# Kernel tuning notes

Hardware: AMD Instinct MI355X
Metric: run time of the kernel (lower is better)

## Reference

```python
import jax, jax.numpy as jnp
import numpy as np

INF = 1e30  # sentinel for 'unreached' cost
MAX_ITERS = 512


def setup_inputs() -> dict:
    key = jax.random.key(0)
    img = jax.random.uniform(key, (3, 2048, 2048), dtype=jnp.float32)
    return {"img": img}


def _sobel_mag(gray):
    # gray: [H,W] -> gradient magnitude [H,W] (the 'processing_filter')
    kx = jnp.array([[-1.0, 0.0, 1.0], [-2.0, 0.0, 2.0], [-1.0, 0.0, 1.0]], gray.dtype)
    k = jnp.stack([kx, kx.T])[:, None]  # [2,1,3,3]
    g = jax.lax.conv_general_dilated(gray[None, None], k, (1, 1), 'SAME')[0]  # [2,H,W]
    return jnp.sqrt(g[0] ** 2 + g[1] ** 2)


def _neighbor_min(c):
    # min over 4-connected neighbors, INF padding at borders
    big_r = jnp.full((1, c.shape[1]), INF, c.dtype)
    big_c = jnp.full((c.shape[0], 1), INF, c.dtype)
    n = jnp.concatenate([big_r, c[:-1]], 0)
    s = jnp.concatenate([c[1:], big_r], 0)
    w = jnp.concatenate([big_c, c[:, :-1]], 1)
    e = jnp.concatenate([c[:, 1:], big_c], 1)
    return jnp.minimum(jnp.minimum(n, s), jnp.minimum(w, e))


def _relax(cost, img):
    # minimax-path (flood-level) relaxation: cost[p] = min(cost[p], max(min_nbr_cost, img[p]))
    return jnp.minimum(cost, jnp.maximum(_neighbor_min(cost), img))


def _watershed2(img, markers):
    # marker-based watershed on topography `img` with labels {1,2}.
    # Label of p = argmin over seed sets of the minimax path cost (flooding level),
    # which matches skimage.segmentation.watershed region assignment (4-connectivity).
    c1 = jnp.where(markers == 1, img, jnp.float32(INF))
    c2 = jnp.where(markers == 2, img, jnp.float32(INF))

    def cond(st):
        _, _, i, ch = st
        return jnp.logical_and(ch, i < MAX_ITERS)

    def body(st):
        c1, c2, i, _ = st
        n1 = _relax(c1, img)
        n2 = _relax(c2, img)
        ch = jnp.logical_or(jnp.any(n1 < c1), jnp.any(n2 < c2))
        return n1, n2, i + 1, ch

    c1, c2, _, _ = jax.lax.while_loop(cond, body, (c1, c2, jnp.int32(0), jnp.bool_(True)))
    return jnp.where(c2 < c1, jnp.float32(2.0), jnp.float32(1.0))


def _forward(img):
    gray = jnp.einsum('chw,c->hw', img, jnp.array([0.2989, 0.587, 0.114], img.dtype))
    filter_res = _sobel_mag(gray)  # [H,W]
    q_hi = jnp.quantile(filter_res, 0.9925)
    q_lo = jnp.quantile(filter_res, 0.9825)
    # torch sets 2 first, then 1, so pixels satisfying both end up as 1
    markers = jnp.where(filter_res <= q_lo, 1, jnp.where(filter_res >= q_hi, 2, 0))
    labels = _watershed2(gray, markers)[None]  # [1,H,W], values in {1,2}
    labels = labels - labels.min()
    return labels / labels.max()


def reference(img):
    return _forward(img)
```

## Files before the change

kernel.cpp:

```cpp
#include <hip/hip_runtime.h>
#include <hip/hip_cooperative_groups.h>

#define HH 2048
#define WW 2048
#define NPX (HH*WW)
#define INFV 1e30f
#define TS 128
#define NT 16
#define NTL 256
#define CY 128

namespace cg = cooperative_groups;

__device__ __forceinline__ void BARL(){
  __builtin_amdgcn_sched_barrier(0);
  asm volatile("s_waitcnt lgkmcnt(0)" ::: "memory");
  __builtin_amdgcn_s_barrier();
  __builtin_amdgcn_sched_barrier(0);
}

__device__ __forceinline__ float sobel_at(const float* __restrict__ g, int y, int x){
  float a00,a01,a02,a10,a12,a20,a21,a22;
  if (y>0 && y<HH-1 && x>0 && x<WW-1){
    const float* p = g + (size_t)(y-1)*WW + x;
    a00=p[-1]; a01=p[0]; a02=p[1];
    p += WW;   a10=p[-1];          a12=p[1];
    p += WW;   a20=p[-1]; a21=p[0]; a22=p[1];
  } else {
    auto at=[&](int yy,int xx)->float{
      return (yy<0||yy>=HH||xx<0||xx>=WW)?0.0f:g[(size_t)yy*WW+xx];
    };
    a00=at(y-1,x-1); a01=at(y-1,x); a02=at(y-1,x+1);
    a10=at(y,  x-1);                a12=at(y,  x+1);
    a20=at(y+1,x-1); a21=at(y+1,x); a22=at(y+1,x+1);
  }
  float gx = __fadd_rn(__fadd_rn(__fsub_rn(a02,a00), __fmul_rn(2.0f,__fsub_rn(a12,a10))), __fsub_rn(a22,a20));
  float gy = __fadd_rn(__fadd_rn(__fsub_rn(a20,a00), __fmul_rn(2.0f,__fsub_rn(a21,a01))), __fsub_rn(a22,a02));
  return sqrtf(__fadd_rn(__fmul_rn(gx,gx),__fmul_rn(gy,gy)));
}

__global__ void gray_kernel(const float* __restrict__ img, float* __restrict__ gray){
  const float* R=img; const float* G=img+NPX; const float* B=img+2*(size_t)NPX;
  for (int i=blockIdx.x*blockDim.x+threadIdx.x; i<NPX; i+=gridDim.x*blockDim.x){
    gray[i] = __fadd_rn(__fadd_rn(__fmul_rn(0.2989f,R[i]),__fmul_rn(0.587f,G[i])),__fmul_rn(0.114f,B[i]));
  }
}

__global__ void sobel_hist1(const float* __restrict__ gray, float* __restrict__ fr,
                            unsigned* __restrict__ hist){
  __shared__ unsigned h[4*2048];
  for (int i=threadIdx.x;i<4*2048;i+=blockDim.x) h[i]=0;
  __syncthreads();
  const int rep=(threadIdx.x&3)*2048;
  for (int i=blockIdx.x*blockDim.x+threadIdx.x; i<NPX; i+=gridDim.x*blockDim.x){
    int y=i>>11, x=i&(WW-1);
    float f=sobel_at(gray,y,x);
    fr[i]=f;
    unsigned key=__float_as_uint(f);
    atomicAdd(&h[rep+(key>>21)],1u);
  }
  __syncthreads();
  for (int i=threadIdx.x;i<2048;i+=blockDim.x){
    unsigned s=h[i]+h[i+2048]+h[i+4096]+h[i+6144];
    if (s) atomicAdd(&hist[i],s);
  }
}

__global__ void hist_l2(const float* __restrict__ fr, const unsigned* __restrict__ sel1,
                        unsigned* __restrict__ hist2){
  __shared__ unsigned h[4*2048];
  __shared__ unsigned sb[4];
  if (threadIdx.x<4) sb[threadIdx.x]=sel1[threadIdx.x];
  for (int i=threadIdx.x;i<4*2048;i+=blockDim.x) h[i]=0;
  __syncthreads();
  for (int i=blockIdx.x*blockDim.x+threadIdx.x; i<NPX; i+=gridDim.x*blockDim.x){
    unsigned key=__float_as_uint(fr[i]);
    unsigned b=key>>21, sub=(key>>10)&0x7FFu;
    #pragma unroll
    for (int k=0;k<4;++k) if (b==sb[k]) atomicAdd(&h[k*2048+sub],1u);
  }
  __syncthreads();
  for (int i=threadIdx.x;i<4*2048;i+=blockDim.x){ unsigned s=h[i]; if (s) atomicAdd(&hist2[i],s); }
}

__global__ void hist_l3(const float* __restrict__ fr, const unsigned* __restrict__ sel1,
                        const unsigned* __restrict__ sel2, unsigned* __restrict__ hist3){
  __shared__ unsigned h[4*1024];
  __shared__ unsigned pf[4];
  if (threadIdx.x<4) pf[threadIdx.x]=(sel1[threadIdx.x]<<11)|sel2[threadIdx.x];
  for (int i=threadIdx.x;i<4*1024;i+=blockDim.x) h[i]=0;
  __syncthreads();
  for (int i=blockIdx.x*blockDim.x+threadIdx.x; i<NPX; i+=gridDim.x*blockDim.x){
    unsigned key=__float_as_uint(fr[i]);
    unsigned p22=key>>10, sub=key&0x3FFu;
    #pragma unroll
    for (int k=0;k<4;++k) if (p22==pf[k]) atomicAdd(&h[k*1024+sub],1u);
  }
  __syncthreads();
  for (int i=threadIdx.x;i<4*1024;i+=blockDim.x){ unsigned s=h[i]; if (s) atomicAdd(&hist3[i],s); }
}

__global__ void scan_l1(const unsigned* __restrict__ hist, unsigned* __restrict__ sel1,
                        unsigned* __restrict__ rem1){
  __shared__ unsigned part[1024];
  const int t=threadIdx.x;
  unsigned a=hist[2*t], b=hist[2*t+1];
  part[t]=a+b; __syncthreads();
  for (int off=1;off<1024;off<<=1){
    unsigned add=(t>=off)?part[t-off]:0u; __syncthreads();
    part[t]+=add; __syncthreads();
  }
  unsigned before=(t>0)?part[t-1]:0u;
  const unsigned R[4]={4120902u,4120903u,4162845u,4162846u};
  unsigned cum=before;
  #pragma unroll
  for (int i=0;i<4;++i) if (R[i]>=cum && R[i]<cum+a){ sel1[i]=2*t;   rem1[i]=R[i]-cum; }
  cum+=a;
  #pragma unroll
  for (int i=0;i<4;++i) if (R[i]>=cum && R[i]<cum+b){ sel1[i]=2*t+1; rem1[i]=R[i]-cum; }
}

__global__ void scan_l2(const unsigned* __restrict__ hist2, const unsigned* __restrict__ rem1,
                        unsigned* __restrict__ sel2, unsigned* __restrict__ rem2){
  __shared__ unsigned part[1024];
  const int t=threadIdx.x;
  for (int i=0;i<4;++i){
    const unsigned* hh=hist2+i*2048;
    unsigned a=hh[2*t], b=hh[2*t+1];
    part[t]=a+b; __syncthreads();
    for (int off=1;off<1024;off<<=1){
      unsigned add=(t>=off)?part[t-off]:0u; __syncthreads();
      part[t]+=add; __syncthreads();
    }
    unsigned before=(t>0)?part[t-1]:0u;
    unsigned r=rem1[i], cum=before;
    if (r>=cum && r<cum+a){ sel2[i]=2*t;   rem2[i]=r-cum; }
    cum+=a;
    if (r>=cum && r<cum+b){ sel2[i]=2*t+1; rem2[i]=r-cum; }
    __syncthreads();
  }
}

__global__ void scan_l3(const unsigned* __restrict__ hist3, const unsigned* __restrict__ sel1,
                        const unsigned* __restrict__ sel2, const unsigned* __restrict__ rem2,
                        float* __restrict__ scal){
  __shared__ unsigned part[1024];
  __shared__ float vals[4];
  const int t=threadIdx.x;
  for (int i=0;i<4;++i){
    unsigned c=hist3[i*1024+t];
    part[t]=c; __syncthreads();
    for (int off=1;off<1024;off<<=1){
      unsigned add=(t>=off)?part[t-off]:0u; __syncthreads();
      part[t]+=add; __syncthreads();
    }
    unsigned before=(t>0)?part[t-1]:0u;
    unsigned r=rem2[i];
    if (r>=before && r<before+c){
      unsigned key=(sel1[i]<<21)|(sel2[i]<<10)|(unsigned)t;
      vals[i]=__uint_as_float(key);
    }
    __syncthreads();
  }
  if (t==0){
    scal[0]=__fadd_rn(__fmul_rn(vals[0],0.25f),__fmul_rn(vals[1],0.75f));
    scal[1]=__fadd_rn(__fmul_rn(vals[2],0.25f),__fmul_rn(vals[3],0.75f));
  }
}

__global__ void init_cost(const float* __restrict__ gray, const float* frbuf,
                          const float* __restrict__ scal,
                          float* c1out, float* __restrict__ c2out){
  const float qlo=scal[0], qhi=scal[1];
  for (int i=blockIdx.x*blockDim.x+threadIdx.x; i<NPX; i+=gridDim.x*blockDim.x){
    float f=frbuf[i];
    float g=gray[i];
    bool m1 = (f<=qlo);
    bool m2 = (!m1) && (f>=qhi);
    c1out[i] = m1 ? g : INFV;
    c2out[i] = (m1|m2) ? g : INFV;
  }
}


#define HSCAN_LR(va,vb,gA,gB,hl) do{ \
  float ql_=gA[j], qh_=va[j]; \
  qh_=fminf(vb[j],fmaxf(gB[j],qh_)); ql_=fmaxf(gB[j],ql_); \
  _Pragma("unroll") \
  for (int d_=1;d_<64;d_<<=1){ \
    float pl_=__shfl_up(ql_,(unsigned)d_), ph_=__shfl_up(qh_,(unsigned)d_); \
    if (c>=d_){ qh_=fminf(qh_,fmaxf(ql_,ph_)); ql_=fmaxf(ql_,pl_); } \
  } \
  float E_=fminf(qh_,fmaxf(ql_,(hl))); \
  float In_=__shfl_up(E_,1u); if(c==0) In_=(hl); \
  float na_=fminf(va[j],fmaxf(gA[j],In_)); if(na_<va[j]){va[j]=na_;ch=true;} \
  float nb_=fminf(vb[j],fmaxf(gB[j],na_)); if(nb_<vb[j]){vb[j]=nb_;ch=true;} \
}while(0)

#define HSCAN_RL(va,vb,gA,gB,hr) do{ \
  float ql_=gB[j], qh_=vb[j]; \
  qh_=fminf(va[j],fmaxf(gA[j],qh_)); ql_=fmaxf(gA[j],ql_); \
  _Pragma("unroll") \
  for (int d_=1;d_<64;d_<<=1){ \
    float pl_=__shfl_down(ql_,(unsigned)d_), ph_=__shfl_down(qh_,(unsigned)d_); \
    if (c+d_<64){ qh_=fminf(qh_,fmaxf(ql_,ph_)); ql_=fmaxf(ql_,pl_); } \
  } \
  float E_=fminf(qh_,fmaxf(ql_,(hr))); \
  float In_=__shfl_down(E_,1u); if(c==63) In_=(hr); \
  float nb_=fminf(vb[j],fmaxf(gB[j],In_)); if(nb_<vb[j]){vb[j]=nb_;ch=true;} \
  float na_=fminf(va[j],fmaxf(gA[j],nb_)); if(na_<va[j]){va[j]=na_;ch=true;} \
}while(0)

#define VCOMP_DN(va,gA,Larr,Harr,XX) { float ql_=gA[0], qh_=va[0]; \
  _Pragma("unroll") for (int jj_=1;jj_<8;++jj_){ qh_=fminf(va[jj_],fmaxf(gA[jj_],qh_)); ql_=fmaxf(gA[jj_],ql_);} \
  Larr[w][XX]=ql_; Harr[w][XX]=qh_; }

#define VCOMP_UP(va,gA,Larr,Harr,XX) { float ql_=gA[7], qh_=va[7]; \
  _Pragma("unroll") for (int jj_=6;jj_>=0;--jj_){ qh_=fminf(va[jj_],fmaxf(gA[jj_],qh_)); ql_=fmaxf(gA[jj_],ql_);} \
  Larr[w][XX]=ql_; Harr[w][XX]=qh_; }

#define VAPPLY_DN(va,gA,Larr,XX) { float In_=Larr[w][XX]; \
  _Pragma("unroll") for (int jj_=0;jj_<8;++jj_){ float nv_=fminf(va[jj_],fmaxf(In_,gA[jj_])); if(nv_<va[jj_]){va[jj_]=nv_;ch=true;} In_=nv_; } }

#define VAPPLY_UP(va,gA,Larr,XX) { float In_=Larr[w][XX]; \
  _Pragma("unroll") for (int jj_=7;jj_>=0;--jj_){ float nv_=fminf(va[jj_],fmaxf(In_,gA[jj_])); if(nv_<va[jj_]){va[jj_]=nv_;ch=true;} In_=nv_; } }

#define CHAIN_DN(Harr,Larr,HT) { float E=HALO[HT][x]; \
  _Pragma("unroll") for (int b_=0;b_<16;++b_){ float I=E; E=fminf(Harr[b_][x],fmaxf(Larr[b_][x],I)); Larr[b_][x]=I; } }

#define CHAIN_UP(Harr,Larr,HB) { float E=HALO[HB][x]; \
  _Pragma("unroll") for (int b_=15;b_>=0;--b_){ float I=E; E=fminf(Harr[b_][x],fmaxf(Larr[b_][x],I)); Larr[b_][x]=I; } }

#define HFIELD(va,vb,IHL,IHR) do{ \
  _Pragma("unroll") \
  for (int j=0;j<8;++j){ \
    const int r_=(w<<3)|j; \
    const float hl=HALO[IHL][r_], hr=HALO[IHR][r_]; \
    { float la_=__shfl_up(vb[j],1u); if(c==0) la_=hl; \
      bool p_=__any((fminf(va[j],fmaxf(la_,ga[j]))<va[j])||(fminf(vb[j],fmaxf(va[j],gb[j]))<vb[j])); \
      if (p_){ HSCAN_LR(va,vb,ga,gb,hl); } } \
    { float ra_=__shfl_down(va[j],1u); if(c==63) ra_=hr; \
      bool p_=__any((fminf(vb[j],fmaxf(ra_,gb[j]))<vb[j])||(fminf(va[j],fmaxf(vb[j],ga[j]))<va[j])); \
      if (p_){ HSCAN_RL(va,vb,ga,gb,hr); } } \
  } \
}while(0)

#define ASTORE(p,v) __hip_atomic_store((p),(v),__ATOMIC_RELAXED,__HIP_MEMORY_SCOPE_AGENT)
#define ALOAD(p)    __hip_atomic_load((p),__ATOMIC_RELAXED,__HIP_MEMORY_SCOPE_AGENT)

#define CYCLE(HV,CUR,NXT) do{ \
  if (hsrc){ \
    if (HV < HALO[harr][hx]){ \
      HALO[harr][hx]=HV; \
      if (harr<4){ if (harr&1) VN2[NXT]=1; else VN1[NXT]=1; } \
      else       { if (harr&1) HN2[NXT]=1; else HN1[NXT]=1; } \
    } \
    HV=ALOAD(hsrc); \
  } \
  const int vn1=VN1[CUR], hn1=HN1[CUR], vn2=VN2[CUR], hn2=HN2[CUR]; \
  if (!(vn1|hn1|vn2|hn2)){ \
    BARL(); \
  } else { \
    if (vn1){ \
      VCOMP_DN(v1a,ga,DNL1,DNH1,x0) VCOMP_DN(v1b,gb,DNL1,DNH1,x0+1) \
      VCOMP_UP(v1a,ga,UPL1,UPH1,x0) VCOMP_UP(v1b,gb,UPL1,UPH1,x0+1) \
    } \
    if (vn2){ \
      VCOMP_DN(v2a,ga,DNL2,DNH2,x0) VCOMP_DN(v2b,gb,DNL2,DNH2,x0+1) \
      VCOMP_UP(v2a,ga,UPL2,UPH2,x0) VCOMP_UP(v2b,gb,UPL2,UPH2,x0+1) \
    } \
    BARL(); \
    if (w<8){ \
      const int x=((w&1)<<6)|c; \
      const bool go = (w>>2) ? (vn2!=0) : (vn1!=0); \
      if (go){ \
        switch(w>>1){ \
          case 0: CHAIN_DN(DNH1,DNL1,0) break; \
          case 1: CHAIN_UP(UPH1,UPL1,2) break; \
          case 2: CHAIN_DN(DNH2,DNL2,1) break; \
          default:CHAIN_UP(UPH2,UPL2,3) break; \
        } \
      } \
    } \
    BARL(); \
    bool chf1=false, chf2=false; \
    if (vn1){ bool ch=false; \
      VAPPLY_DN(v1a,ga,DNL1,x0) VAPPLY_DN(v1b,gb,DNL1,x0+1) \
      VAPPLY_UP(v1a,ga,UPL1,x0) VAPPLY_UP(v1b,gb,UPL1,x0+1) \
      if (ch){ chf1=true; HN1[NXT]=1; } \
    } \
    if (hn1){ bool ch=false; \
      HFIELD(v1a,v1b,4,6); \
      if (ch){ chf1=true; VN1[NXT]=1; } \
    } \
    if (vn2){ bool ch=false; \
      VAPPLY_DN(v2a,ga,DNL2,x0) VAPPLY_DN(v2b,gb,DNL2,x0+1) \
      VAPPLY_UP(v2a,ga,UPL2,x0) VAPPLY_UP(v2b,gb,UPL2,x0+1) \
      if (ch){ chf2=true; HN2[NXT]=1; } \
    } \
    if (hn2){ bool ch=false; \
      HFIELD(v2a,v2b,5,7); \
      if (ch){ chf2=true; VN2[NXT]=1; } \
    } \
    if (chf1|chf2){ \
      if (w==0){ const int eb=(tile*4+0)*128; \
        if(chf1){ ASTORE(EB1+eb+x0,v1a[0]); ASTORE(EB1+eb+x0+1,v1b[0]); } \
        if(chf2){ ASTORE(EB2+eb+x0,v2a[0]); ASTORE(EB2+eb+x0+1,v2b[0]); } } \
      if (w==15){ const int eb=(tile*4+1)*128; \
        if(chf1){ ASTORE(EB1+eb+x0,v1a[7]); ASTORE(EB1+eb+x0+1,v1b[7]); } \
        if(chf2){ ASTORE(EB2+eb+x0,v2a[7]); ASTORE(EB2+eb+x0+1,v2b[7]); } } \
      if (c==0){ const int eb=(tile*4+2)*128+(w<<3); \
        _Pragma("unroll") \
        for (int j=0;j<8;++j){ if(chf1)ASTORE(EB1+eb+j,v1a[j]); if(chf2)ASTORE(EB2+eb+j,v2a[j]); } } \
      if (c==63){ const int eb=(tile*4+3)*128+(w<<3); \
        _Pragma("unroll") \
        for (int j=0;j<8;++j){ if(chf1)ASTORE(EB1+eb+j,v1b[j]); if(chf2)ASTORE(EB2+eb+j,v2b[j]); } } \
      wflag=1; \
    } \
    if (tid==0){ VN1[CUR]=0; HN1[CUR]=0; VN2[CUR]=0; HN2[CUR]=0; } \
    BARL(); \
  } \
}while(0)

__global__ void __launch_bounds__(1024,4)
ws_solve(float* __restrict__ c1g, const float* __restrict__ grayg, float* outg,
         int* __restrict__ flagIt)
{
  __shared__ float DNL1[16][128], DNH1[16][128], DNL2[16][128], DNH2[16][128];
  __shared__ float UPL1[16][128], UPH1[16][128], UPL2[16][128], UPH2[16][128];
  __shared__ float HALO[8][128];
  __shared__ int VN1[2],HN1[2],VN2[2],HN2[2];
  __shared__ int wflag;
  cg::grid_group grid = cg::this_grid();
  const int tid=threadIdx.x, w=tid>>6, c=tid&63;
  const int xcd=blockIdx.x&7, idx=blockIdx.x>>3;
  const int tx=((xcd&3)<<2)|(idx&3), ty=((xcd>>2)<<3)|(idx>>2);
  const int tile=ty*NT+tx;
  const int by=ty*TS, bx=tx*TS, x0=c<<1;
  float* EB1=outg;
  float* EB2=outg+(NTL*4*128);

  const int hx=tid&127, harr=tid>>7;
  const float* hsrc=nullptr;
  {
    const float* EB=(harr&1)?EB2:EB1;
    switch(harr>>1){
      case 0: if (ty>0)    hsrc=EB+((tile-NT)*4+1)*128+hx; break;
      case 1: if (ty<NT-1) hsrc=EB+((tile+NT)*4+0)*128+hx; break;
      case 2: if (tx>0)    hsrc=EB+((tile-1)*4+3)*128+hx;  break;
      default:if (tx<NT-1) hsrc=EB+((tile+1)*4+2)*128+hx;  break;
    }
  }

  float v1a[8],v1b[8],v2a[8],v2b[8],ga[8],gb[8];
  {
    size_t base=(size_t)(by+(w<<3))*WW + bx + x0;
    #pragma unroll
    for (int j=0;j<8;++j){
      float2 t1=*(const float2*)(c1g+base);
      float2 t2=*(const float2*)(outg+base);
      float2 tg=*(const float2*)(grayg+base);
      v1a[j]=t1.x; v1b[j]=t1.y; v2a[j]=t2.x; v2b[j]=t2.y; ga[j]=tg.x; gb[j]=tg.y;
      base+=(size_t)WW;
    }
  }
  grid.sync();

  if (w==0){ const int eb=(tile*4+0)*128;
    ASTORE(EB1+eb+x0,v1a[0]); ASTORE(EB1+eb+x0+1,v1b[0]);
    ASTORE(EB2+eb+x0,v2a[0]); ASTORE(EB2+eb+x0+1,v2b[0]); }
  if (w==15){ const int eb=(tile*4+1)*128;
    ASTORE(EB1+eb+x0,v1a[7]); ASTORE(EB1+eb+x0+1,v1b[7]);
    ASTORE(EB2+eb+x0,v2a[7]); ASTORE(EB2+eb+x0+1,v2b[7]); }
  if (c==0){ const int eb=(tile*4+2)*128+(w<<3);
    #pragma unroll
    for (int j=0;j<8;++j){ ASTORE(EB1+eb+j,v1a[j]); ASTORE(EB2+eb+j,v2a[j]); } }
  if (c==63){ const int eb=(tile*4+3)*128+(w<<3);
    #pragma unroll
    for (int j=0;j<8;++j){ ASTORE(EB1+eb+j,v1b[j]); ASTORE(EB2+eb+j,v2b[j]); } }
  HALO[harr][hx]=INFV;
  if (tid==0){ VN1[0]=1;HN1[0]=1;VN2[0]=1;HN2[0]=1;
               VN1[1]=0;HN1[1]=0;VN2[1]=0;HN2[1]=0; wflag=0; }
  __threadfence();
  grid.sync();

  float hvA=INFV, hvB=INFV;
  if (hsrc){ hvA=ALOAD(hsrc); hvB=ALOAD(hsrc); }

  for (int win=0; win<48; ++win){
    for (int cyc=0; cyc<CY; cyc+=2){
      CYCLE(hvA,0,1);
      CYCLE(hvB,1,0);
    }
    if (tid==0 && wflag) atomicMax(flagIt,win+1);
    __threadfence();
    grid.sync();
    int fv=ALOAD(flagIt);
    if (fv<=win) break;
    if (tid==0) wflag=0;
    __syncthreads();
  }
  {
    size_t base=(size_t)(by+(w<<3))*WW + bx + x0;
    #pragma unroll
    for (int j=0;j<8;++j){
      float2 o; o.x=(v2a[j]<v1a[j])?1.0f:0.0f; o.y=(v2b[j]<v1b[j])?1.0f:0.0f;
      *(float2*)(outg+base)=o;
      base+=(size_t)WW;
    }
  }
}

extern "C" void kernel_launch(void* const* d_in, const int* in_sizes, int n_in,
                              void* d_out, int out_size, void* d_ws, size_t ws_size,
                              hipStream_t stream)
{
  const float* img=(const float*)d_in[0];
  float* out=(float*)d_out;
  char* wsb=(char*)d_ws;
  float* gray=(float*)wsb;
  float* c1  =(float*)(wsb + (size_t)NPX*4);
  unsigned* meta=(unsigned*)(wsb + (size_t)NPX*8);
  float* c2 = out;

  unsigned* hist1=meta;
  unsigned* hist2=meta+2048;
  unsigned* hist3=meta+10240;
  unsigned* sel1 =meta+14336;
  unsigned* rem1 =meta+14340;
  unsigned* sel2 =meta+14344;
  unsigned* rem2 =meta+14348;
  float*    scal =(float*)(meta+14352);
  int*      flagIt=(int*)(meta+14354);

  hipMemsetAsync(meta, 0, 14355*sizeof(unsigned), stream);
  hipLaunchKernelGGL(gray_kernel, dim3(4096), dim3(256), 0, stream, img, gray);
  hipLaunchKernelGGL(sobel_hist1, dim3(1024), dim3(256), 0, stream, gray, c1, hist1);
  hipLaunchKernelGGL(scan_l1, dim3(1), dim3(1024), 0, stream, hist1, sel1, rem1);
  hipLaunchKernelGGL(hist_l2, dim3(1024), dim3(256), 0, stream, c1, sel1, hist2);
  hipLaunchKernelGGL(scan_l2, dim3(1), dim3(1024), 0, stream, hist2, rem1, sel2, rem2);
  hipLaunchKernelGGL(hist_l3, dim3(1024), dim3(256), 0, stream, c1, sel1, sel2, hist3);
  hipLaunchKernelGGL(scan_l3, dim3(1), dim3(1024), 0, stream, hist3, sel1, sel2, rem2, scal);
  hipLaunchKernelGGL(init_cost, dim3(4096), dim3(256), 0, stream, gray, c1, scal, c1, c2);

  void* args[]={ (void*)&c1,(void*)&gray,(void*)&out,(void*)&flagIt };
  (void)hipLaunchCooperativeKernel(ws_solve, dim3(NTL), dim3(1024), args, 0, stream);
}
```

Measured before the change: 609.5 us.

## Add overlapping-tile local pre-solve pass before cooperative watershed flood

Adds a non-cooperative tile_solve kernel that loads 128x128 windows with 32-pixel overlap, runs up to 64 local relaxation cycles in shared memory and registers, and writes back the central 64x64 region. The aim is to converge most of the cost field locally before the cooperative grid-synchronized solver runs. It also shrinks the cycles per window (CY 128 to 32) and raises the window cap, so the grid-wide convergence check fires more often. The cost is an extra full-image kernel pass with redundant halo work. The write-back also relies on the local minimax values staying valid upper bounds, which they do because they are still real path costs.

```diff
diff --git a/kernel.cpp b/kernel.cpp
--- a/kernel.cpp
+++ b/kernel.cpp
@@ -8,7 +8,7 @@
 #define TS 128
 #define NT 16
 #define NTL 256
-#define CY 128
+#define CY 32
 
 namespace cg = cooperative_groups;
 
@@ -247,6 +247,103 @@
 
 #define ASTORE(p,v) __hip_atomic_store((p),(v),__ATOMIC_RELAXED,__HIP_MEMORY_SCOPE_AGENT)
 #define ALOAD(p)    __hip_atomic_load((p),__ATOMIC_RELAXED,__HIP_MEMORY_SCOPE_AGENT)
+
+__global__ void __launch_bounds__(1024,4)
+tile_solve(float* __restrict__ c1g, float* __restrict__ cg, const float* __restrict__ grayg)
+{
+  __shared__ float DNL1[16][128], DNH1[16][128], DNL2[16][128], DNH2[16][128];
+  __shared__ float UPL1[16][128], UPH1[16][128], UPL2[16][128], UPH2[16][128];
+  __shared__ float HALO[8][128];
+  __shared__ int VN1[2],HN1[2],VN2[2],HN2[2];
+  const int tid=threadIdx.x, w=tid>>6, c=tid&63;
+  const int oty=blockIdx.x>>5, otx=blockIdx.x&31;
+  const int wy0=oty*64-32, wx0=otx*64-32, x0=c<<1;
+  HALO[tid>>7][tid&127]=INFV;
+  if (tid==0){ VN1[0]=1;HN1[0]=1;VN2[0]=1;HN2[0]=1;
+               VN1[1]=0;HN1[1]=0;VN2[1]=0;HN2[1]=0; }
+  float v1a[8],v1b[8],v2a[8],v2b[8],ga[8],gb[8];
+  const int gx=wx0+x0;
+  const bool cok=(gx>=0)&&(gx+1<WW);
+  #pragma unroll
+  for (int j=0;j<8;++j){
+    const int gy=wy0+(w<<3)+j;
+    const bool rok=(gy>=0)&&(gy<HH);
+    if (rok&&cok){
+      const size_t b=(size_t)gy*WW+gx;
+      float2 t1=*(const float2*)(c1g+b);
+      float2 t2=*(const float2*)(cg+b);
+      float2 tg=*(const float2*)(grayg+b);
+      v1a[j]=t1.x; v1b[j]=t1.y; v2a[j]=t2.x; v2b[j]=t2.y; ga[j]=tg.x; gb[j]=tg.y;
+    } else if (rok){
+      const bool aok=(gx>=0)&&(gx<WW), bok=(gx+1>=0)&&(gx+1<WW);
+      const size_t b=(size_t)gy*WW;
+      v1a[j]=aok?c1g[b+gx]:INFV;   v1b[j]=bok?c1g[b+gx+1]:INFV;
+      v2a[j]=aok?cg [b+gx]:INFV;   v2b[j]=bok?cg [b+gx+1]:INFV;
+      ga [j]=aok?grayg[b+gx]:INFV; gb [j]=bok?grayg[b+gx+1]:INFV;
+    } else {
+      v1a[j]=INFV;v1b[j]=INFV;v2a[j]=INFV;v2b[j]=INFV;ga[j]=INFV;gb[j]=INFV;
+    }
+  }
+  __syncthreads();
+  for (int cyc=0; cyc<64; ++cyc){
+    const int cur=cyc&1, nxt=cur^1;
+    const int vn1=VN1[cur], hn1=HN1[cur], vn2=VN2[cur], hn2=HN2[cur];
+    if (!(vn1|hn1|vn2|hn2)) break;
+    if (vn1){
+      VCOMP_DN(v1a,ga,DNL1,DNH1,x0) VCOMP_DN(v1b,gb,DNL1,DNH1,x0+1)
+      VCOMP_UP(v1a,ga,UPL1,UPH1,x0) VCOMP_UP(v1b,gb,UPL1,UPH1,x0+1)
+    }
+    if (vn2){
+      VCOMP_DN(v2a,ga,DNL2,DNH2,x0) VCOMP_DN(v2b,gb,DNL2,DNH2,x0+1)
+      VCOMP_UP(v2a,ga,UPL2,UPH2,x0) VCOMP_UP(v2b,gb,UPL2,UPH2,x0+1)
+    }
+    __syncthreads();
+    if (w<8){
+      const int x=((w&1)<<6)|c;
+      const bool go=(w>>2)?(vn2!=0):(vn1!=0);
+      if (go){
+        switch(w>>1){
+          case 0: CHAIN_DN(DNH1,DNL1,0) break;
+          case 1: CHAIN_UP(UPH1,UPL1,2) break;
+          case 2: CHAIN_DN(DNH2,DNL2,1) break;
+          default:CHAIN_UP(UPH2,UPL2,3) break;
+        }
+      }
+    }
+    __syncthreads();
+    if (vn1){ bool ch=false;
+      VAPPLY_DN(v1a,ga,DNL1,x0) VAPPLY_DN(v1b,gb,DNL1,x0+1)
+      VAPPLY_UP(v1a,ga,UPL1,x0) VAPPLY_UP(v1b,gb,UPL1,x0+1)
+      if (ch) HN1[nxt]=1;
+    }
+    if (hn1){ bool ch=false;
+      HFIELD(v1a,v1b,4,6);
+      if (ch) VN1[nxt]=1;
+    }
+    if (vn2){ bool ch=false;
+      VAPPLY_DN(v2a,ga,DNL2,x0) VAPPLY_DN(v2b,gb,DNL2,x0+1)
+      VAPPLY_UP(v2a,ga,UPL2,x0) VAPPLY_UP(v2b,gb,UPL2,x0+1)
+      if (ch) HN2[nxt]=1;
+    }
+    if (hn2){ bool ch=false;
+      HFIELD(v2a,v2b,5,7);
+      if (ch) VN2[nxt]=1;
+    }
+    if (tid==0){ VN1[cur]=0; HN1[cur]=0; VN2[cur]=0; HN2[cur]=0; }
+    __syncthreads();
+  }
+  if (w>=4 && w<12 && c>=16 && c<48){
+    #pragma unroll
+    for (int j=0;j<8;++j){
+      const int gy=wy0+(w<<3)+j;
+      const size_t b=(size_t)gy*WW+gx;
+      float2 o1; o1.x=v1a[j]; o1.y=v1b[j];
+      float2 o2; o2.x=v2a[j]; o2.y=v2b[j];
+      *(float2*)(c1g+b)=o1;
+      *(float2*)(cg +b)=o2;
+    }
+  }
+}
 
 #define CYCLE(HV,CUR,NXT) do{ \
   if (hsrc){ \
@@ -387,7 +484,7 @@
   float hvA=INFV, hvB=INFV;
   if (hsrc){ hvA=ALOAD(hsrc); hvB=ALOAD(hsrc); }
 
-  for (int win=0; win<48; ++win){
+  for (int win=0; win<96; ++win){
     for (int cyc=0; cyc<CY; cyc+=2){
       CYCLE(hvA,0,1);
       CYCLE(hvB,1,0);
@@ -443,6 +540,8 @@
   hipLaunchKernelGGL(scan_l3, dim3(1), dim3(1024), 0, stream, hist3, sel1, sel2, rem2, scal);
   hipLaunchKernelGGL(init_cost, dim3(4096), dim3(256), 0, stream, gray, c1, scal, c1, c2);
 
+  hipLaunchKernelGGL(tile_solve, dim3(1024), dim3(1024), 0, stream, c1, c2, gray);
+
   void* args[]={ (void*)&c1,(void*)&gray,(void*)&out,(void*)&flagIt };
   (void)hipLaunchCooperativeKernel(ws_solve, dim3(NTL), dim3(1024), args, 0, stream);
 }
```

After: 562.1 us. 1.08x faster.
